# Performance work log

Hardware: AMD Instinct MI355X
Metric: run time of the kernel (lower is better)

Reference implementation:

```python
import jax, jax.numpy as jnp
import numpy as np

GROUP = 16  # quantization group size along in_features
EPS = 1e-5


def _qlora_linear(x, qw, sc, b, la, lb):
    # qw: [O, I] int4 codes; sc: [O, I//GROUP] fp32 group scales
    O, I = qw.shape
    w = (qw.astype(jnp.float32).reshape(O, I // GROUP, GROUP) * sc[:, :, None]).reshape(O, I)
    base = x @ w.T + b                      # [N, O]
    lora = (x @ la.T) @ lb.T                # [N, R] @ [R, O]
    return base + lora


def _layernorm(x, g, b):
    m = jnp.mean(x, axis=-1, keepdims=True)
    v = jnp.var(x, axis=-1, keepdims=True)
    return (x - m) * jax.lax.rsqrt(v + EPS) * g + b


def setup_inputs() -> dict:
    key = jax.random.key(0)
    ks = jax.random.split(key, 8)
    N, D, R, L = 16384, 1024, 32, 18  # tokens, BIGNET_DIM, lora_dim, num linears
    x = jax.random.normal(ks[0], (N, D), jnp.float32)
    qw = jax.random.randint(ks[1], (L, D, D), -8, 8, jnp.int32)  # signed 4-bit codes
    scales = jax.random.uniform(ks[2], (L, D, D // GROUP), jnp.float32, 0.005, 0.02)
    bias = 0.01 * jax.random.normal(ks[3], (L, D), jnp.float32)
    la = 0.001 * jax.random.normal(ks[4], (L, R, D), jnp.float32)
    lb = 0.01 * jax.random.normal(ks[5], (L, D, R), jnp.float32)
    ln_g = jnp.ones((5, D), jnp.float32) + 0.1 * jax.random.normal(ks[6], (5, D), jnp.float32)
    ln_b = 0.01 * jax.random.normal(ks[7], (5, D), jnp.float32)
    return {"x": x, "qw": qw, "scales": scales, "bias": bias,
            "la": la, "lb": lb, "ln_g": ln_g, "ln_b": ln_b}


def reference(x, qw, scales, bias, la, lb, ln_g, ln_b):
    h = x
    for blk in range(6):
        y = h
        for j in range(3):
            i = blk * 3 + j
            y = _qlora_linear(y, qw[i], scales[i], bias[i], la[i], lb[i])
            if j < 2:
                y = jax.nn.relu(y)
        h = y + h  # residual
        if blk < 5:
            h = _layernorm(h, ln_g[blk], ln_b[blk])
    return h
```

## Files before the change

### kernel.cpp

```cpp
#include <hip/hip_runtime.h>

#define DIM 1024
#define NTOK 16384

typedef __attribute__((ext_vector_type(8))) _Float16 f16x8;
typedef __attribute__((ext_vector_type(4))) _Float16 f16x4;
typedef __attribute__((ext_vector_type(4))) float f32x4;

__device__ __forceinline__ void gload_lds16(const void* g, void* l) {
  __builtin_amdgcn_global_load_lds(
      (const __attribute__((address_space(1))) void*)g,
      (__attribute__((address_space(3))) void*)l, 16, 0, 0);
}

__device__ __forceinline__ f16x8 ldsr(const char* smem, int byteoff) {
  return *(const f16x8*)(smem + byteoff);
}

__device__ __forceinline__ f32x4 mfma16(f16x8 a, f16x8 b, f32x4 c) {
  return __builtin_amdgcn_mfma_f32_16x16x32_f16(a, b, c, 0, 0, 0);
}

__global__ __launch_bounds__(256) void cvt_kernel(const float* __restrict__ in,
                                                  _Float16* __restrict__ out) {
  const int i = blockIdx.x * 256 + threadIdx.x;
  float4 v = reinterpret_cast<const float4*>(in)[i];
  f16x4 o;
  o[0] = (_Float16)v.x;
  o[1] = (_Float16)v.y;
  o[2] = (_Float16)v.z;
  o[3] = (_Float16)v.w;
  *reinterpret_cast<f16x4*>(&out[(size_t)i * 4]) = o;
}

__global__ __launch_bounds__(256) void build_weff(const int* __restrict__ qw,
                                                  const float* __restrict__ scales,
                                                  const float* __restrict__ la,
                                                  const float* __restrict__ lb,
                                                  _Float16* __restrict__ W) {
  __shared__ float la_s[32][256];
  __shared__ float lb_s[32][32];
  const int kt = blockIdx.x;
  const int ot = blockIdx.y;
  const int l = blockIdx.z;
  const int tid = threadIdx.x;

  for (int idx = tid; idx < 2048; idx += 256) {
    const int r = idx >> 6, c4 = (idx & 63) * 4;
    *(float4*)&la_s[r][c4] =
        *(const float4*)&la[((size_t)l * 32 + r) * DIM + kt * 256 + c4];
  }
  {
    const int o = tid >> 3, r4 = (tid & 7) * 4;
    *(float4*)&lb_s[o][r4] =
        *(const float4*)&lb[((size_t)l * DIM + ot * 32 + o) * 32 + r4];
  }
  __syncthreads();

  const int kq = tid & 63;
  const int os = tid >> 6;
  const int k0 = kq * 4;
  const int kg = kt * 256 + k0;
  const size_t rb = (size_t)l * DIM + ot * 32 + os * 8;

  int4 q[8];
  float sc[8];
#pragma unroll
  for (int oi = 0; oi < 8; ++oi) {
    q[oi] = *(const int4*)&qw[(rb + oi) * DIM + kg];
    sc[oi] = scales[(rb + oi) * 64 + (kg >> 4)];
  }

  float acc[8][4];
#pragma unroll
  for (int a = 0; a < 8; ++a)
#pragma unroll
    for (int b = 0; b < 4; ++b) acc[a][b] = 0.f;

#pragma unroll
  for (int r4 = 0; r4 < 8; ++r4) {
    float lbr[8][4];
#pragma unroll
    for (int oi = 0; oi < 8; ++oi) {
      const float4 v = *(const float4*)&lb_s[os * 8 + oi][r4 * 4];
      lbr[oi][0] = v.x;
      lbr[oi][1] = v.y;
      lbr[oi][2] = v.z;
      lbr[oi][3] = v.w;
    }
#pragma unroll
    for (int rr = 0; rr < 4; ++rr) {
      const float4 a4 = *(const float4*)&la_s[r4 * 4 + rr][k0];
#pragma unroll
      for (int oi = 0; oi < 8; ++oi) {
        acc[oi][0] = fmaf(lbr[oi][rr], a4.x, acc[oi][0]);
        acc[oi][1] = fmaf(lbr[oi][rr], a4.y, acc[oi][1]);
        acc[oi][2] = fmaf(lbr[oi][rr], a4.z, acc[oi][2]);
        acc[oi][3] = fmaf(lbr[oi][rr], a4.w, acc[oi][3]);
      }
    }
  }

#pragma unroll
  for (int oi = 0; oi < 8; ++oi) {
    f16x4 o4;
    o4[0] = (_Float16)(fmaf((float)q[oi].x, sc[oi], acc[oi][0]));
    o4[1] = (_Float16)(fmaf((float)q[oi].y, sc[oi], acc[oi][1]));
    o4[2] = (_Float16)(fmaf((float)q[oi].z, sc[oi], acc[oi][2]));
    o4[3] = (_Float16)(fmaf((float)q[oi].w, sc[oi], acc[oi][3]));
    *(f16x4*)&W[(rb + oi) * DIM + kg] = o4;
  }
}

#define ST_NONE ((void)0)
#define VM_NONE ((void)0)
#define VM4 asm volatile("s_waitcnt vmcnt(4)" ::: "memory")
#define VM0 asm volatile("s_waitcnt vmcnt(0)" ::: "memory")

#define RDA(BUF, FM, KS) \
  ldsr(smem, (((BUF)*2 + wm) << 14) + (((FM)*16 + r16) << 7) + (cks ^ ((KS) << 6)))
#define RDB(BUF, FN, KS)                                                        \
  ldsr(smem, 65536 + (((BUF)*2 + (wn >> 1)) << 14) +                            \
                 ((((wn & 1) * 64) + (FN)*16 + r16) << 7) + (cks ^ ((KS) << 6)))

#define PH(QQ, BUFC, STAGE, VMASM)                                          \
  {                                                                         \
    if ((QQ) == 0) {                                                        \
      _Pragma("unroll") for (int fn = 0; fn < 4; ++fn) {                    \
        bf[fn][0] = RDB(BUFC, fn, 0);                                       \
        bf[fn][1] = RDB(BUFC, fn, 1);                                       \
      }                                                                     \
    }                                                                       \
    f16x8 a00 = RDA(BUFC, 2 * (QQ), 0);                                     \
    f16x8 a01 = RDA(BUFC, 2 * (QQ), 1);                                     \
    f16x8 a10 = RDA(BUFC, 2 * (QQ) + 1, 0);                                 \
    f16x8 a11 = RDA(BUFC, 2 * (QQ) + 1, 1);                                 \
    STAGE;                                                                  \
    asm volatile("" ::: "memory");                                          \
    __builtin_amdgcn_s_barrier();                                           \
    asm volatile("s_waitcnt lgkmcnt(0)" ::: "memory");                      \
    __builtin_amdgcn_s_setprio(1);                                          \
    _Pragma("unroll") for (int fn = 0; fn < 4; ++fn) {                      \
      acc[2 * (QQ)][fn] = mfma16(a00, bf[fn][0], acc[2 * (QQ)][fn]);        \
      acc[2 * (QQ)][fn] = mfma16(a01, bf[fn][1], acc[2 * (QQ)][fn]);        \
      acc[2 * (QQ) + 1][fn] = mfma16(a10, bf[fn][0], acc[2 * (QQ) + 1][fn]); \
      acc[2 * (QQ) + 1][fn] = mfma16(a11, bf[fn][1], acc[2 * (QQ) + 1][fn]); \
    }                                                                       \
    __builtin_amdgcn_s_setprio(0);                                          \
    VMASM;                                                                  \
    asm volatile("" ::: "memory");                                          \
    __builtin_amdgcn_s_barrier();                                           \
  }

template <int MODE>
__global__ __launch_bounds__(512, 2) void qgemm(const _Float16* __restrict__ X,
                                                const _Float16* __restrict__ W,
                                                const float* __restrict__ bias,
                                                const _Float16* __restrict__ RES,
                                                void* __restrict__ OUT) {
  extern __shared__ char smem[];

  const int tid = threadIdx.x;
  const int wave = tid >> 6;
  const int lane = tid & 63;
  const int wm = wave >> 2;
  const int wn = wave & 3;
  const int bn = blockIdx.x;
  const int bm = blockIdx.y;

  const int r16 = lane & 15;
  const int cks = ((lane >> 4) * 16) ^ ((lane & 7) << 4);

  const int srl = lane >> 3;
  const int scs = ((lane & 7) ^ srl) << 3;

  f32x4 acc[8][4];
#pragma unroll
  for (int i = 0; i < 8; ++i)
#pragma unroll
    for (int j = 0; j < 4; ++j)
#pragma unroll
      for (int r = 0; r < 4; ++r) acc[i][j][r] = 0.f;

  auto stageA = [&](int buf, int h, int t) {
    const _Float16* g =
        X + (size_t)(bm * 256 + h * 128 + wave * 16 + srl) * DIM + t * 64 + scs;
    char* d = smem + (((buf * 2 + h) << 14) + wave * 2048);
    gload_lds16(g, d);
    gload_lds16(g + 8 * DIM, d + 1024);
  };
  auto stageB = [&](int buf, int h, int t) {
    const _Float16* g =
        W + (size_t)(bn * 256 + h * 128 + wave * 16 + srl) * DIM + t * 64 + scs;
    char* d = smem + (65536 + ((buf * 2 + h) << 14) + wave * 2048);
    gload_lds16(g, d);
    gload_lds16(g + 8 * DIM, d + 1024);
  };

  stageA(0, 0, 0);
  stageA(0, 1, 0);
  stageB(0, 0, 0);
  stageB(0, 1, 0);
  stageB(1, 0, 1);
  stageB(1, 1, 1);
  VM4;
  __builtin_amdgcn_s_barrier();

  f16x8 bf[4][2];

  for (int i = 0; i < 7; ++i) {
    const int t0 = 2 * i, t1 = 2 * i + 1;
    PH(0, 0, stageA(1, 0, t1), VM_NONE)
    PH(1, 0, stageA(1, 1, t1), VM_NONE)
    PH(2, 0, stageB(0, 0, t0 + 2), VM_NONE)
    PH(3, 0, stageB(0, 1, t0 + 2), VM4)
    PH(0, 1, stageA(0, 0, t0 + 2), VM_NONE)
    PH(1, 1, stageA(0, 1, t0 + 2), VM_NONE)
    PH(2, 1, stageB(1, 0, t1 + 2), VM_NONE)
    PH(3, 1, stageB(1, 1, t1 + 2), VM4)
  }
  PH(0, 0, stageA(1, 0, 15), VM_NONE)
  PH(1, 0, stageA(1, 1, 15), VM_NONE)
  PH(2, 0, ST_NONE, VM_NONE)
  PH(3, 0, ST_NONE, VM0)
  PH(0, 1, ST_NONE, VM_NONE)
  PH(1, 1, ST_NONE, VM_NONE)
  PH(2, 1, ST_NONE, VM_NONE)
  PH(3, 1, ST_NONE, VM_NONE)

  const int row0 = bm * 256 + wm * 128;
  const int col0 = bn * 256 + wn * 64;
  const int rg = (lane >> 4) * 4;
  float bv[4];
#pragma unroll
  for (int fn = 0; fn < 4; ++fn) bv[fn] = bias[col0 + fn * 16 + r16];

#pragma unroll
  for (int fm = 0; fm < 8; ++fm) {
#pragma unroll
    for (int fn = 0; fn < 4; ++fn) {
      const int col = col0 + fn * 16 + r16;
#pragma unroll
      for (int r = 0; r < 4; ++r) {
        const int row = row0 + fm * 16 + rg + r;
        float v = acc[fm][fn][r] + bv[fn];
        if (MODE == 0) {
          v = fmaxf(v, 0.f);
          ((_Float16*)OUT)[(size_t)row * DIM + col] = (_Float16)v;
        } else {
          v += (float)RES[(size_t)row * DIM + col];
          if (MODE == 1)
            ((_Float16*)OUT)[(size_t)row * DIM + col] = (_Float16)v;
          else
            ((float*)OUT)[(size_t)row * DIM + col] = v;
        }
      }
    }
  }
}

__global__ __launch_bounds__(256) void ln_kernel(const _Float16* __restrict__ in,
                                                 const float* __restrict__ g,
                                                 const float* __restrict__ b,
                                                 _Float16* __restrict__ out) {
  const int row = blockIdx.x;
  const int tid = threadIdx.x;
  const _Float16* rp = in + (size_t)row * DIM;

  f16x4 raw = reinterpret_cast<const f16x4*>(rp)[tid];
  float v0 = (float)raw[0], v1 = (float)raw[1], v2 = (float)raw[2], v3 = (float)raw[3];
  float s = v0 + v1 + v2 + v3;
  float sq = v0 * v0 + v1 * v1 + v2 * v2 + v3 * v3;
#pragma unroll
  for (int off = 32; off > 0; off >>= 1) {
    s += __shfl_down(s, off);
    sq += __shfl_down(sq, off);
  }
  __shared__ float ss[4], sq4[4];
  if ((tid & 63) == 0) {
    ss[tid >> 6] = s;
    sq4[tid >> 6] = sq;
  }
  __syncthreads();
  s = ss[0] + ss[1] + ss[2] + ss[3];
  sq = sq4[0] + sq4[1] + sq4[2] + sq4[3];
  const float mean = s * (1.f / DIM);
  const float var = sq * (1.f / DIM) - mean * mean;
  const float inv = rsqrtf(var + 1e-5f);

  float4 gv = reinterpret_cast<const float4*>(g)[tid];
  float4 bv = reinterpret_cast<const float4*>(b)[tid];
  f16x4 o;
  o[0] = (_Float16)((v0 - mean) * inv * gv.x + bv.x);
  o[1] = (_Float16)((v1 - mean) * inv * gv.y + bv.y);
  o[2] = (_Float16)((v2 - mean) * inv * gv.z + bv.z);
  o[3] = (_Float16)((v3 - mean) * inv * gv.w + bv.w);
  *reinterpret_cast<f16x4*>(&out[(size_t)row * DIM + tid * 4]) = o;
}


extern "C" void kernel_launch(void* const* d_in, const int* in_sizes, int n_in,
                              void* d_out, int out_size, void* d_ws, size_t ws_size,
                              hipStream_t stream) {
  const float* x = (const float*)d_in[0];
  const int* qw = (const int*)d_in[1];
  const float* scales = (const float*)d_in[2];
  const float* bias = (const float*)d_in[3];
  const float* la = (const float*)d_in[4];
  const float* lb = (const float*)d_in[5];
  const float* ln_g = (const float*)d_in[6];
  const float* ln_b = (const float*)d_in[7];

  char* ws = (char*)d_ws;
  const size_t WEFF_BYTES = (size_t)18 * DIM * DIM * 2;
  const size_t ACT_BYTES = (size_t)NTOK * DIM * 2;
  _Float16* Weff = (_Float16*)ws;
  _Float16* bufA = (_Float16*)(ws + WEFF_BYTES);
  _Float16* bufB = (_Float16*)(ws + WEFF_BYTES + ACT_BYTES);
  _Float16* bufC = (_Float16*)(ws + WEFF_BYTES + 2 * ACT_BYTES);

  const int LDS_BYTES = 131072;
  (void)hipFuncSetAttribute((const void*)&qgemm<0>,
                            hipFuncAttributeMaxDynamicSharedMemorySize, LDS_BYTES);
  (void)hipFuncSetAttribute((const void*)&qgemm<1>,
                            hipFuncAttributeMaxDynamicSharedMemorySize, LDS_BYTES);
  (void)hipFuncSetAttribute((const void*)&qgemm<2>,
                            hipFuncAttributeMaxDynamicSharedMemorySize, LDS_BYTES);

  cvt_kernel<<<NTOK * DIM / 1024, 256, 0, stream>>>(x, bufA);
  build_weff<<<dim3(4, 32, 18), 256, 0, stream>>>(qw, scales, la, lb, Weff);

  const dim3 ggrid(DIM / 256, NTOK / 256);
  for (int blk = 0; blk < 6; ++blk) {
    const int i0 = blk * 3;
    const size_t wstep = (size_t)DIM * DIM;
    qgemm<0><<<ggrid, 512, LDS_BYTES, stream>>>(bufA, Weff + (size_t)i0 * wstep,
                                                bias + i0 * DIM, nullptr, bufB);
    qgemm<0><<<ggrid, 512, LDS_BYTES, stream>>>(bufB, Weff + (size_t)(i0 + 1) * wstep,
                                                bias + (i0 + 1) * DIM, nullptr, bufC);
    if (blk < 5) {
      qgemm<1><<<ggrid, 512, LDS_BYTES, stream>>>(bufC, Weff + (size_t)(i0 + 2) * wstep,
                                                  bias + (i0 + 2) * DIM, bufA, bufB);
      ln_kernel<<<NTOK, 256, 0, stream>>>(bufB, ln_g + blk * DIM, ln_b + blk * DIM, bufA);
    } else {
      qgemm<2><<<ggrid, 512, LDS_BYTES, stream>>>(bufC, Weff + (size_t)(i0 + 2) * wstep,
                                                  bias + (i0 + 2) * DIM, bufA, d_out);
    }
  }
}
```

Measured before the change: 810.8 us.

## Switch GEMM to 32x32x16 MFMA tiles and read LoRA B from global

```diff
diff --git a/kernel.cpp b/kernel.cpp
--- a/kernel.cpp
+++ b/kernel.cpp
@@ -6,6 +6,7 @@
 typedef __attribute__((ext_vector_type(8))) _Float16 f16x8;
 typedef __attribute__((ext_vector_type(4))) _Float16 f16x4;
 typedef __attribute__((ext_vector_type(4))) float f32x4;
+typedef __attribute__((ext_vector_type(16))) float f32x16;
 
 __device__ __forceinline__ void gload_lds16(const void* g, void* l) {
   __builtin_amdgcn_global_load_lds(
@@ -17,8 +18,8 @@
   return *(const f16x8*)(smem + byteoff);
 }
 
-__device__ __forceinline__ f32x4 mfma16(f16x8 a, f16x8 b, f32x4 c) {
-  return __builtin_amdgcn_mfma_f32_16x16x32_f16(a, b, c, 0, 0, 0);
+__device__ __forceinline__ f32x16 mfma32(f16x8 a, f16x8 b, f32x16 c) {
+  return __builtin_amdgcn_mfma_f32_32x32x16_f16(a, b, c, 0, 0, 0);
 }
 
 __global__ __launch_bounds__(256) void cvt_kernel(const float* __restrict__ in,
@@ -39,7 +40,6 @@
                                                   const float* __restrict__ lb,
                                                   _Float16* __restrict__ W) {
   __shared__ float la_s[32][256];
-  __shared__ float lb_s[32][32];
   const int kt = blockIdx.x;
   const int ot = blockIdx.y;
   const int l = blockIdx.z;
@@ -50,15 +50,10 @@
     *(float4*)&la_s[r][c4] =
         *(const float4*)&la[((size_t)l * 32 + r) * DIM + kt * 256 + c4];
   }
-  {
-    const int o = tid >> 3, r4 = (tid & 7) * 4;
-    *(float4*)&lb_s[o][r4] =
-        *(const float4*)&lb[((size_t)l * DIM + ot * 32 + o) * 32 + r4];
-  }
   __syncthreads();
 
   const int kq = tid & 63;
-  const int os = tid >> 6;
+  const int os = __builtin_amdgcn_readfirstlane(tid >> 6);
   const int k0 = kq * 4;
   const int kg = kt * 256 + k0;
   const size_t rb = (size_t)l * DIM + ot * 32 + os * 8;
@@ -82,7 +77,7 @@
     float lbr[8][4];
 #pragma unroll
     for (int oi = 0; oi < 8; ++oi) {
-      const float4 v = *(const float4*)&lb_s[os * 8 + oi][r4 * 4];
+      const float4 v = *(const float4*)&lb[(rb + oi) * 32 + r4 * 4];
       lbr[oi][0] = v.x;
       lbr[oi][1] = v.y;
       lbr[oi][2] = v.z;
@@ -118,34 +113,37 @@
 #define VM0 asm volatile("s_waitcnt vmcnt(0)" ::: "memory")
 
 #define RDA(BUF, FM, KS) \
-  ldsr(smem, (((BUF)*2 + wm) << 14) + (((FM)*16 + r16) << 7) + (cks ^ ((KS) << 6)))
+  ldsr(smem, (((BUF)*2 + wm) << 14) + (((FM)*32 + r32) << 7) + (cA ^ ((KS) << 5)))
 #define RDB(BUF, FN, KS)                                                        \
   ldsr(smem, 65536 + (((BUF)*2 + (wn >> 1)) << 14) +                            \
-                 ((((wn & 1) * 64) + (FN)*16 + r16) << 7) + (cks ^ ((KS) << 6)))
+                 ((((wn & 1) * 64) + (FN)*32 + r32) << 7) + (cA ^ ((KS) << 5)))
 
 #define PH(QQ, BUFC, STAGE, VMASM)                                          \
   {                                                                         \
     if ((QQ) == 0) {                                                        \
-      _Pragma("unroll") for (int fn = 0; fn < 4; ++fn) {                    \
-        bf[fn][0] = RDB(BUFC, fn, 0);                                       \
-        bf[fn][1] = RDB(BUFC, fn, 1);                                       \
+      _Pragma("unroll") for (int fn = 0; fn < 2; ++fn) {                    \
+        _Pragma("unroll") for (int ks = 0; ks < 4; ++ks) {                  \
+          bf[fn][ks] = RDB(BUFC, fn, ks);                                   \
+        }                                                                   \
       }                                                                     \
     }                                                                       \
-    f16x8 a00 = RDA(BUFC, 2 * (QQ), 0);                                     \
-    f16x8 a01 = RDA(BUFC, 2 * (QQ), 1);                                     \
-    f16x8 a10 = RDA(BUFC, 2 * (QQ) + 1, 0);                                 \
-    f16x8 a11 = RDA(BUFC, 2 * (QQ) + 1, 1);                                 \
+    f16x8 a0 = RDA(BUFC, QQ, 0);                                            \
+    f16x8 a1 = RDA(BUFC, QQ, 1);                                            \
+    f16x8 a2 = RDA(BUFC, QQ, 2);                                            \
+    f16x8 a3 = RDA(BUFC, QQ, 3);                                            \
     STAGE;                                                                  \
     asm volatile("" ::: "memory");                                          \
     __builtin_amdgcn_s_barrier();                                           \
     asm volatile("s_waitcnt lgkmcnt(0)" ::: "memory");                      \
     __builtin_amdgcn_s_setprio(1);                                          \
-    _Pragma("unroll") for (int fn = 0; fn < 4; ++fn) {                      \
-      acc[2 * (QQ)][fn] = mfma16(a00, bf[fn][0], acc[2 * (QQ)][fn]);        \
-      acc[2 * (QQ)][fn] = mfma16(a01, bf[fn][1], acc[2 * (QQ)][fn]);        \
-      acc[2 * (QQ) + 1][fn] = mfma16(a10, bf[fn][0], acc[2 * (QQ) + 1][fn]); \
-      acc[2 * (QQ) + 1][fn] = mfma16(a11, bf[fn][1], acc[2 * (QQ) + 1][fn]); \
-    }                                                                       \
+    acc[QQ][0] = mfma32(a0, bf[0][0], acc[QQ][0]);                          \
+    acc[QQ][1] = mfma32(a0, bf[1][0], acc[QQ][1]);                          \
+    acc[QQ][0] = mfma32(a1, bf[0][1], acc[QQ][0]);                          \
+    acc[QQ][1] = mfma32(a1, bf[1][1], acc[QQ][1]);                          \
+    acc[QQ][0] = mfma32(a2, bf[0][2], acc[QQ][0]);                          \
+    acc[QQ][1] = mfma32(a2, bf[1][2], acc[QQ][1]);                          \
+    acc[QQ][0] = mfma32(a3, bf[0][3], acc[QQ][0]);                          \
+    acc[QQ][1] = mfma32(a3, bf[1][3], acc[QQ][1]);                          \
     __builtin_amdgcn_s_setprio(0);                                          \
     VMASM;                                                                  \
     asm volatile("" ::: "memory");                                          \
@@ -168,19 +166,19 @@
   const int bn = blockIdx.x;
   const int bm = blockIdx.y;
 
-  const int r16 = lane & 15;
-  const int cks = ((lane >> 4) * 16) ^ ((lane & 7) << 4);
+  const int r32 = lane & 31;
+  const int cA = ((lane >> 5) << 4) ^ ((lane & 7) << 4);
 
   const int srl = lane >> 3;
   const int scs = ((lane & 7) ^ srl) << 3;
 
-  f32x4 acc[8][4];
-#pragma unroll
-  for (int i = 0; i < 8; ++i)
-#pragma unroll
-    for (int j = 0; j < 4; ++j)
-#pragma unroll
-      for (int r = 0; r < 4; ++r) acc[i][j][r] = 0.f;
+  f32x16 acc[4][2];
+#pragma unroll
+  for (int i = 0; i < 4; ++i)
+#pragma unroll
+    for (int j = 0; j < 2; ++j)
+#pragma unroll
+      for (int r = 0; r < 16; ++r) acc[i][j][r] = 0.f;
 
   auto stageA = [&](int buf, int h, int t) {
     const _Float16* g =
@@ -206,7 +204,7 @@
   VM4;
   __builtin_amdgcn_s_barrier();
 
-  f16x8 bf[4][2];
+  f16x8 bf[2][4];
 
   for (int i = 0; i < 7; ++i) {
     const int t0 = 2 * i, t1 = 2 * i + 1;
@@ -228,22 +226,19 @@
   PH(2, 1, ST_NONE, VM_NONE)
   PH(3, 1, ST_NONE, VM_NONE)
 
-  const int row0 = bm * 256 + wm * 128;
-  const int col0 = bn * 256 + wn * 64;
-  const int rg = (lane >> 4) * 4;
-  float bv[4];
-#pragma unroll
-  for (int fn = 0; fn < 4; ++fn) bv[fn] = bias[col0 + fn * 16 + r16];
-
-#pragma unroll
-  for (int fm = 0; fm < 8; ++fm) {
-#pragma unroll
-    for (int fn = 0; fn < 4; ++fn) {
-      const int col = col0 + fn * 16 + r16;
-#pragma unroll
-      for (int r = 0; r < 4; ++r) {
-        const int row = row0 + fm * 16 + rg + r;
-        float v = acc[fm][fn][r] + bv[fn];
+  const int row_b = bm * 256 + wm * 128 + 4 * (lane >> 5);
+  const int col_b = bn * 256 + wn * 64 + r32;
+  float bvv[2] = {bias[col_b], bias[col_b + 32]};
+
+#pragma unroll
+  for (int fm = 0; fm < 4; ++fm) {
+#pragma unroll
+    for (int fn = 0; fn < 2; ++fn) {
+      const int col = col_b + fn * 32;
+#pragma unroll
+      for (int reg = 0; reg < 16; ++reg) {
+        const int row = row_b + fm * 32 + (reg & 3) + 8 * (reg >> 2);
+        float v = acc[fm][fn][reg] + bvv[fn];
         if (MODE == 0) {
           v = fmaxf(v, 0.f);
           ((_Float16*)OUT)[(size_t)row * DIM + col] = (_Float16)v;
```

Measured after the change: 902.2 us. 1.11x slower.

## Shrink GEMM K-tile to 32 with double-buffered 64KB static LDS

Applied to the files above, without the earlier changes.

```diff
diff --git a/kernel.cpp b/kernel.cpp
--- a/kernel.cpp
+++ b/kernel.cpp
@@ -112,44 +112,55 @@
   }
 }
 
-#define ST_NONE ((void)0)
-#define VM_NONE ((void)0)
-#define VM4 asm volatile("s_waitcnt vmcnt(4)" ::: "memory")
+#define MEMBAR asm volatile("" ::: "memory")
 #define VM0 asm volatile("s_waitcnt vmcnt(0)" ::: "memory")
 
-#define RDA(BUF, FM, KS) \
-  ldsr(smem, (((BUF)*2 + wm) << 14) + (((FM)*16 + r16) << 7) + (cks ^ ((KS) << 6)))
-#define RDB(BUF, FN, KS)                                                        \
-  ldsr(smem, 65536 + (((BUF)*2 + (wn >> 1)) << 14) +                            \
-                 ((((wn & 1) * 64) + (FN)*16 + r16) << 7) + (cks ^ ((KS) << 6)))
-
-#define PH(QQ, BUFC, STAGE, VMASM)                                          \
-  {                                                                         \
-    if ((QQ) == 0) {                                                        \
-      _Pragma("unroll") for (int fn = 0; fn < 4; ++fn) {                    \
-        bf[fn][0] = RDB(BUFC, fn, 0);                                       \
-        bf[fn][1] = RDB(BUFC, fn, 1);                                       \
-      }                                                                     \
-    }                                                                       \
-    f16x8 a00 = RDA(BUFC, 2 * (QQ), 0);                                     \
-    f16x8 a01 = RDA(BUFC, 2 * (QQ), 1);                                     \
-    f16x8 a10 = RDA(BUFC, 2 * (QQ) + 1, 0);                                 \
-    f16x8 a11 = RDA(BUFC, 2 * (QQ) + 1, 1);                                 \
-    STAGE;                                                                  \
-    asm volatile("" ::: "memory");                                          \
-    __builtin_amdgcn_s_barrier();                                           \
-    asm volatile("s_waitcnt lgkmcnt(0)" ::: "memory");                      \
-    __builtin_amdgcn_s_setprio(1);                                          \
-    _Pragma("unroll") for (int fn = 0; fn < 4; ++fn) {                      \
-      acc[2 * (QQ)][fn] = mfma16(a00, bf[fn][0], acc[2 * (QQ)][fn]);        \
-      acc[2 * (QQ)][fn] = mfma16(a01, bf[fn][1], acc[2 * (QQ)][fn]);        \
-      acc[2 * (QQ) + 1][fn] = mfma16(a10, bf[fn][0], acc[2 * (QQ) + 1][fn]); \
-      acc[2 * (QQ) + 1][fn] = mfma16(a11, bf[fn][1], acc[2 * (QQ) + 1][fn]); \
-    }                                                                       \
-    __builtin_amdgcn_s_setprio(0);                                          \
-    VMASM;                                                                  \
-    asm volatile("" ::: "memory");                                          \
-    __builtin_amdgcn_s_barrier();                                           \
+#define RDA(BUF, FM) \
+  ldsr(smem, ((BUF) << 14) + ((wm * 128 + (FM)*16 + r16) << 6) + cA)
+#define RDB(BUF, FN) \
+  ldsr(smem, 32768 + ((BUF) << 14) + ((wn * 64 + (FN)*16 + r16) << 6) + cA)
+
+#define PH0(T, C)                                                        \
+  {                                                                      \
+    bf[0] = RDB(C, 0);                                                   \
+    bf[1] = RDB(C, 1);                                                   \
+    bf[2] = RDB(C, 2);                                                   \
+    bf[3] = RDB(C, 3);                                                   \
+    f16x8 a0 = RDA(C, 0), a1 = RDA(C, 1), a2 = RDA(C, 2), a3 = RDA(C, 3); \
+    if ((T) + 1 < 32) stageA((C) ^ 1, (T) + 1);                          \
+    MEMBAR;                                                              \
+    __builtin_amdgcn_s_barrier();                                        \
+    asm volatile("s_waitcnt lgkmcnt(0)" ::: "memory");                   \
+    __builtin_amdgcn_s_setprio(1);                                       \
+    _Pragma("unroll") for (int fn = 0; fn < 4; ++fn) {                   \
+      acc[0][fn] = mfma16(a0, bf[fn], acc[0][fn]);                       \
+      acc[1][fn] = mfma16(a1, bf[fn], acc[1][fn]);                       \
+      acc[2][fn] = mfma16(a2, bf[fn], acc[2][fn]);                       \
+      acc[3][fn] = mfma16(a3, bf[fn], acc[3][fn]);                       \
+    }                                                                    \
+    __builtin_amdgcn_s_setprio(0);                                       \
+    MEMBAR;                                                              \
+    __builtin_amdgcn_s_barrier();                                        \
+  }
+
+#define PH1(T, C)                                                        \
+  {                                                                      \
+    f16x8 a4 = RDA(C, 4), a5 = RDA(C, 5), a6 = RDA(C, 6), a7 = RDA(C, 7); \
+    if ((T) + 1 < 32) stageB((C) ^ 1, (T) + 1);                          \
+    MEMBAR;                                                              \
+    __builtin_amdgcn_s_barrier();                                        \
+    asm volatile("s_waitcnt lgkmcnt(0)" ::: "memory");                   \
+    __builtin_amdgcn_s_setprio(1);                                       \
+    _Pragma("unroll") for (int fn = 0; fn < 4; ++fn) {                   \
+      acc[4][fn] = mfma16(a4, bf[fn], acc[4][fn]);                       \
+      acc[5][fn] = mfma16(a5, bf[fn], acc[5][fn]);                       \
+      acc[6][fn] = mfma16(a6, bf[fn], acc[6][fn]);                       \
+      acc[7][fn] = mfma16(a7, bf[fn], acc[7][fn]);                       \
+    }                                                                    \
+    __builtin_amdgcn_s_setprio(0);                                       \
+    if ((T) + 1 < 32) VM0;                                               \
+    MEMBAR;                                                              \
+    __builtin_amdgcn_s_barrier();                                        \
   }
 
 template <int MODE>
@@ -158,7 +169,7 @@
                                                 const float* __restrict__ bias,
                                                 const _Float16* __restrict__ RES,
                                                 void* __restrict__ OUT) {
-  extern __shared__ char smem[];
+  __shared__ char smem[65536];
 
   const int tid = threadIdx.x;
   const int wave = tid >> 6;
@@ -169,10 +180,11 @@
   const int bm = blockIdx.y;
 
   const int r16 = lane & 15;
-  const int cks = ((lane >> 4) * 16) ^ ((lane & 7) << 4);
-
-  const int srl = lane >> 3;
-  const int scs = ((lane & 7) ^ srl) << 3;
+  const int kgrp = lane >> 4;
+  const int cA = ((kgrp ^ ((r16 >> 1) & 3)) << 4);
+
+  const int scol = ((lane & 3) ^ ((lane >> 3) & 3)) * 8;
+  const int srow = lane >> 2;
 
   f32x4 acc[8][4];
 #pragma unroll
@@ -182,51 +194,33 @@
 #pragma unroll
       for (int r = 0; r < 4; ++r) acc[i][j][r] = 0.f;
 
-  auto stageA = [&](int buf, int h, int t) {
-    const _Float16* g =
-        X + (size_t)(bm * 256 + h * 128 + wave * 16 + srl) * DIM + t * 64 + scs;
-    char* d = smem + (((buf * 2 + h) << 14) + wave * 2048);
+  auto stageA = [&](int buf, int t) {
+    const _Float16* g = X + (size_t)(bm * 256 + wave * 16 + srow) * DIM + t * 32 + scol;
+    char* d = smem + (buf << 14) + wave * 1024;
     gload_lds16(g, d);
-    gload_lds16(g + 8 * DIM, d + 1024);
+    gload_lds16(g + (size_t)128 * DIM, d + 8192);
   };
-  auto stageB = [&](int buf, int h, int t) {
-    const _Float16* g =
-        W + (size_t)(bn * 256 + h * 128 + wave * 16 + srl) * DIM + t * 64 + scs;
-    char* d = smem + (65536 + ((buf * 2 + h) << 14) + wave * 2048);
+  auto stageB = [&](int buf, int t) {
+    const _Float16* g = W + (size_t)(bn * 256 + wave * 16 + srow) * DIM + t * 32 + scol;
+    char* d = smem + 32768 + (buf << 14) + wave * 1024;
     gload_lds16(g, d);
-    gload_lds16(g + 8 * DIM, d + 1024);
+    gload_lds16(g + (size_t)128 * DIM, d + 8192);
   };
 
-  stageA(0, 0, 0);
-  stageA(0, 1, 0);
-  stageB(0, 0, 0);
-  stageB(0, 1, 0);
-  stageB(1, 0, 1);
-  stageB(1, 1, 1);
-  VM4;
+  stageA(0, 0);
+  stageB(0, 0);
+  VM0;
   __builtin_amdgcn_s_barrier();
 
-  f16x8 bf[4][2];
-
-  for (int i = 0; i < 7; ++i) {
+  f16x8 bf[4];
+
+  for (int i = 0; i < 16; ++i) {
     const int t0 = 2 * i, t1 = 2 * i + 1;
-    PH(0, 0, stageA(1, 0, t1), VM_NONE)
-    PH(1, 0, stageA(1, 1, t1), VM_NONE)
-    PH(2, 0, stageB(0, 0, t0 + 2), VM_NONE)
-    PH(3, 0, stageB(0, 1, t0 + 2), VM4)
-    PH(0, 1, stageA(0, 0, t0 + 2), VM_NONE)
-    PH(1, 1, stageA(0, 1, t0 + 2), VM_NONE)
-    PH(2, 1, stageB(1, 0, t1 + 2), VM_NONE)
-    PH(3, 1, stageB(1, 1, t1 + 2), VM4)
-  }
-  PH(0, 0, stageA(1, 0, 15), VM_NONE)
-  PH(1, 0, stageA(1, 1, 15), VM_NONE)
-  PH(2, 0, ST_NONE, VM_NONE)
-  PH(3, 0, ST_NONE, VM0)
-  PH(0, 1, ST_NONE, VM_NONE)
-  PH(1, 1, ST_NONE, VM_NONE)
-  PH(2, 1, ST_NONE, VM_NONE)
-  PH(3, 1, ST_NONE, VM_NONE)
+    PH0(t0, 0)
+    PH1(t0, 0)
+    PH0(t1, 1)
+    PH1(t1, 1)
+  }
 
   const int row0 = bm * 256 + wm * 128;
   const int col0 = bn * 256 + wn * 64;
@@ -319,14 +313,6 @@
   _Float16* bufB = (_Float16*)(ws + WEFF_BYTES + ACT_BYTES);
   _Float16* bufC = (_Float16*)(ws + WEFF_BYTES + 2 * ACT_BYTES);
 
-  const int LDS_BYTES = 131072;
-  (void)hipFuncSetAttribute((const void*)&qgemm<0>,
-                            hipFuncAttributeMaxDynamicSharedMemorySize, LDS_BYTES);
-  (void)hipFuncSetAttribute((const void*)&qgemm<1>,
-                            hipFuncAttributeMaxDynamicSharedMemorySize, LDS_BYTES);
-  (void)hipFuncSetAttribute((const void*)&qgemm<2>,
-                            hipFuncAttributeMaxDynamicSharedMemorySize, LDS_BYTES);
-
   cvt_kernel<<<NTOK * DIM / 1024, 256, 0, stream>>>(x, bufA);
   build_weff<<<dim3(4, 32, 18), 256, 0, stream>>>(qw, scales, la, lb, Weff);
 
@@ -334,17 +320,17 @@
   for (int blk = 0; blk < 6; ++blk) {
     const int i0 = blk * 3;
     const size_t wstep = (size_t)DIM * DIM;
-    qgemm<0><<<ggrid, 512, LDS_BYTES, stream>>>(bufA, Weff + (size_t)i0 * wstep,
-                                                bias + i0 * DIM, nullptr, bufB);
-    qgemm<0><<<ggrid, 512, LDS_BYTES, stream>>>(bufB, Weff + (size_t)(i0 + 1) * wstep,
-                                                bias + (i0 + 1) * DIM, nullptr, bufC);
+    qgemm<0><<<ggrid, 512, 0, stream>>>(bufA, Weff + (size_t)i0 * wstep,
+                                        bias + i0 * DIM, nullptr, bufB);
+    qgemm<0><<<ggrid, 512, 0, stream>>>(bufB, Weff + (size_t)(i0 + 1) * wstep,
+                                        bias + (i0 + 1) * DIM, nullptr, bufC);
     if (blk < 5) {
-      qgemm<1><<<ggrid, 512, LDS_BYTES, stream>>>(bufC, Weff + (size_t)(i0 + 2) * wstep,
-                                                  bias + (i0 + 2) * DIM, bufA, bufB);
+      qgemm<1><<<ggrid, 512, 0, stream>>>(bufC, Weff + (size_t)(i0 + 2) * wstep,
+                                          bias + (i0 + 2) * DIM, bufA, bufB);
       ln_kernel<<<NTOK, 256, 0, stream>>>(bufB, ln_g + blk * DIM, ln_b + blk * DIM, bufA);
     } else {
-      qgemm<2><<<ggrid, 512, LDS_BYTES, stream>>>(bufC, Weff + (size_t)(i0 + 2) * wstep,
-                                                  bias + (i0 + 2) * DIM, bufA, d_out);
+      qgemm<2><<<ggrid, 512, 0, stream>>>(bufC, Weff + (size_t)(i0 + 2) * wstep,
+                                          bias + (i0 + 2) * DIM, bufA, d_out);
     }
   }
 }
```

Result: slower. 979.6 us (+20.8%).
